# Performance work log

Measured on AMD Instinct MI355X. Metric: run time of the kernel, lower is better.

The kernel has to match this reference:

```python
import jax, jax.numpy as jnp
import numpy as np

E = 1024       # embedding_dim
HQ = 16        # num_q_heads
G = 4          # group_size
HK = HQ // G   # num_kv_heads = 4
D = E // HQ    # q_head_dim = 64
B, N = 2, 2048


def setup_inputs() -> dict:
    key = jax.random.key(0)
    kx, kq, kk, kv, ko = jax.random.split(key, 5)
    scale = 0.02
    return {
        "x": jax.random.normal(kx, (B, N, E), dtype=jnp.float32),
        # weights stored as (in, out); torch Linear computes x @ W.T, equivalent math
        "Wq": jax.random.normal(kq, (E, E), dtype=jnp.float32) * scale,
        "Wk": jax.random.normal(kk, (E, E // G), dtype=jnp.float32) * scale,
        "Wv": jax.random.normal(kv, (E, E // G), dtype=jnp.float32) * scale,
        "Wo": jax.random.normal(ko, (E, E), dtype=jnp.float32) * scale,
    }


def reference(x, Wq, Wk, Wv, Wo):
    b, n, _ = x.shape
    q = x @ Wq                      # (b, n, E)
    k = x @ Wk                      # (b, n, HK*D)
    v = x @ Wv                      # (b, n, HK*D)
    # 'b n (h d) -> b h n d' then 'b (h g) n d -> b g h n d'  (h outer, g inner)
    q = q.reshape(b, n, HQ, D).transpose(0, 2, 1, 3)          # (b, HQ, n, D)
    q = q.reshape(b, HK, G, n, D).transpose(0, 2, 1, 3, 4)    # (b, G, HK, n, D)
    k = k.reshape(b, n, HK, D).transpose(0, 2, 1, 3)          # (b, HK, n, D)
    v = v.reshape(b, n, HK, D).transpose(0, 2, 1, 3)          # (b, HK, n, D)

    scores = jnp.einsum('bghnd,bhsd->bghns', q, k) / jnp.sqrt(jnp.float32(D))
    causal = jnp.triu(jnp.ones((n, n), dtype=bool), k=1)      # True above diagonal
    scores = jnp.where(causal[None, None, None], -jnp.inf, scores)
    probs = jax.nn.softmax(scores, axis=-1)                   # dropout p=0 -> no-op
    out = jnp.einsum('bghns,bhsd->bghnd', probs, v)           # (b, G, HK, n, D)
    # 'b g h n d -> b n (h g) d -> b n (h g d)'
    out = out.transpose(0, 3, 2, 1, 4).reshape(b, n, E)
    return out @ Wo
```

## Files before the change

kernel.cpp:

```cpp
#include <hip/hip_runtime.h>
#include <hip/hip_bf16.h>
#include <math.h>

#define Bsz 2
#define Nseq 2048
#define Edim 1024
#define HQ 16
#define HK 4
#define Dh 64
#define ROWS (Bsz * Nseq)
#define QKVW 1536
#define SCL 0.1803368801111244f

typedef __attribute__((ext_vector_type(8))) short short8;
typedef __attribute__((ext_vector_type(4))) float f32x4;

__device__ __forceinline__ ushort f2bf_u(float f) {
    union { __hip_bfloat16 h; ushort u; } c;
    c.h = __float2bfloat16(f);
    return c.u;
}
__device__ __forceinline__ unsigned bfpk(float lo, float hi) {
    return ((unsigned)f2bf_u(hi) << 16) | (unsigned)f2bf_u(lo);
}

__device__ __forceinline__ void gld16(const void* g, void* l) {
    __builtin_amdgcn_global_load_lds(
        (const __attribute__((address_space(1))) unsigned*)g,
        (__attribute__((address_space(3))) unsigned*)l, 16, 0, 0);
}

__global__ __launch_bounds__(256) void castx(const float* __restrict__ x,
                                             ushort* __restrict__ xb) {
    size_t i = ((size_t)blockIdx.x * 256 + threadIdx.x) * 8;
    float4 a = *(const float4*)(x + i);
    float4 c = *(const float4*)(x + i + 4);
    short8 v;
    v[0] = f2bf_u(a.x); v[1] = f2bf_u(a.y); v[2] = f2bf_u(a.z); v[3] = f2bf_u(a.w);
    v[4] = f2bf_u(c.x); v[5] = f2bf_u(c.y); v[6] = f2bf_u(c.z); v[7] = f2bf_u(c.w);
    *(short8*)(xb + i) = v;
}

__global__ __launch_bounds__(256) void tcastAll(const float* __restrict__ Wq,
                                                const float* __restrict__ Wk,
                                                const float* __restrict__ Wv,
                                                const float* __restrict__ Wo,
                                                ushort* __restrict__ WqkvT,
                                                ushort* __restrict__ WoT) {
    __shared__ float tle[32][33];
    int bid = blockIdx.x;
    const float* src; ushort* dst; int N;
    if (bid < 1024)      { src = Wq; dst = WqkvT;                          N = 1024; }
    else if (bid < 1280) { src = Wk; dst = WqkvT + (size_t)1024 * 1024;    N = 256;  bid -= 1024; }
    else if (bid < 1536) { src = Wv; dst = WqkvT + (size_t)1280 * 1024;    N = 256;  bid -= 1280; }
    else                 { src = Wo; dst = WoT;                            N = 1024; bid -= 1536; }
    int nj = N >> 5;
    int j0 = (bid % nj) * 32, k0 = (bid / nj) * 32;
    int tx = threadIdx.x & 31, ty = threadIdx.x >> 5;
#pragma unroll
    for (int i = ty; i < 32; i += 8)
        tle[i][tx] = src[(size_t)(k0 + i) * N + j0 + tx];
    __syncthreads();
#pragma unroll
    for (int i = ty; i < 32; i += 8)
        dst[(size_t)(j0 + i) * 1024 + k0 + tx] = f2bf_u(tle[tx][i]);
}

template<int WRITE_BF16>
__global__ __launch_bounds__(256) void gemm_bt(const ushort* __restrict__ A,
                                               const ushort* __restrict__ BT,
                                               void* __restrict__ Cout,
                                               int M, int N, int K) {
    __shared__ __attribute__((aligned(16))) ushort As[2][4][128][8];
    __shared__ __attribute__((aligned(16))) ushort Bs[2][4][64][8];
    const int tid = threadIdx.x;
    const int l = tid & 63, li = l & 15, lg = l >> 4;
    const int w = tid >> 6;
    const int wr = w >> 1, wc = w & 1;
    const int row0 = blockIdx.y * 128, col0 = blockIdx.x * 64;

    f32x4 acc[4][2];
#pragma unroll
    for (int i = 0; i < 4; ++i)
#pragma unroll
        for (int j = 0; j < 2; ++j) {
            acc[i][j][0] = 0.f; acc[i][j][1] = 0.f;
            acc[i][j][2] = 0.f; acc[i][j][3] = 0.f;
        }

    const int nk = K >> 5;

#define G_STAGE(buf, kk)                                                        \
    {                                                                           \
        int k0 = (kk) << 5;                                                     \
        _Pragma("unroll")                                                       \
        for (int i = 0; i < 3; ++i) {                                           \
            int id = w + i * 4;                                                 \
            if (id < 8) {                                                       \
                int g = id >> 1, h = id & 1;                                    \
                gld16(A + (size_t)(row0 + h * 64 + l) * K + k0 + g * 8,         \
                      &As[buf][g][h * 64][0]);                                  \
            } else {                                                            \
                int g = id - 8;                                                 \
                gld16(BT + (size_t)(col0 + l) * K + k0 + g * 8,                 \
                      &Bs[buf][g][0][0]);                                       \
            }                                                                   \
        }                                                                       \
    }

    G_STAGE(0, 0);
    __syncthreads();
    int buf = 0;
    for (int kk = 0; kk < nk; ++kk) {
        if (kk + 1 < nk) G_STAGE(buf ^ 1, kk + 1);
        short8 af[4], bfr[2];
#pragma unroll
        for (int mt = 0; mt < 4; ++mt)
            af[mt] = *(const short8*)&As[buf][lg][wr * 64 + mt * 16 + li][0];
#pragma unroll
        for (int nt = 0; nt < 2; ++nt)
            bfr[nt] = *(const short8*)&Bs[buf][lg][wc * 32 + nt * 16 + li][0];
#pragma unroll
        for (int mt = 0; mt < 4; ++mt)
#pragma unroll
            for (int nt = 0; nt < 2; ++nt)
                acc[mt][nt] = __builtin_amdgcn_mfma_f32_16x16x32_bf16(
                    af[mt], bfr[nt], acc[mt][nt], 0, 0, 0);
        __syncthreads();
        buf ^= 1;
    }
#undef G_STAGE

    if (WRITE_BF16) {
        ushort* C = (ushort*)Cout;
#pragma unroll
        for (int mt = 0; mt < 4; ++mt)
#pragma unroll
            for (int r = 0; r < 4; ++r) {
                int rg = row0 + wr * 64 + mt * 16 + lg * 4 + r;
#pragma unroll
                for (int nt = 0; nt < 2; ++nt)
                    C[(size_t)rg * N + col0 + wc * 32 + nt * 16 + li] =
                        f2bf_u(acc[mt][nt][r]);
            }
    } else {
        float* C = (float*)Cout;
#pragma unroll
        for (int mt = 0; mt < 4; ++mt)
#pragma unroll
            for (int r = 0; r < 4; ++r) {
                int rg = row0 + wr * 64 + mt * 16 + lg * 4 + r;
#pragma unroll
                for (int nt = 0; nt < 2; ++nt)
                    C[(size_t)rg * N + col0 + wc * 32 + nt * 16 + li] =
                        acc[mt][nt][r];
            }
    }
}

__global__ __launch_bounds__(256) void attn_mfma(const ushort* __restrict__ qkv,
                                                 ushort* __restrict__ o) {
    __shared__ __attribute__((aligned(16))) char smem[40960];
    ushort (*Ks)[8][64][8] = (ushort (*)[8][64][8])smem;
    unsigned (*VtD)[2048]  = (unsigned (*)[2048])(smem + 16384);
    ushort (*Ps)[8][16][8] = (ushort (*)[8][16][8])(smem + 32768);

    const int tid = threadIdx.x;
    const int l = tid & 63, li = l & 15, lg = l >> 4;
    const int w = tid >> 6;
    const int bx = blockIdx.x;
    const int hq = blockIdx.y, b = blockIdx.z, hk = hq >> 2;

    const int kp = 2 * (tid & 31), d0v = (tid >> 5) * 8;
    const int gv = kp >> 3, prv = (kp & 7) >> 1;

    const ushort* base  = qkv + (size_t)b * Nseq * QKVW;
    const ushort* vbase = base + 1280 + hk * 64 + d0v;
    const int qloc = w * 16 + li;

    for (int hseg = 0; hseg < 2; ++hseg) {
        const int qt = hseg ? (31 - bx) : bx;
        const int r0 = qt * 64;

        short8 q8[2];
#pragma unroll
        for (int c = 0; c < 2; ++c)
            q8[c] = *(const short8*)(base + (size_t)(r0 + qloc) * QKVW +
                                     hq * 64 + (c * 4 + lg) * 8);

#pragma unroll
        for (int i = 0; i < 2; ++i) {
            int g = w + i * 4;
            gld16(base + (size_t)l * QKVW + 1024 + hk * 64 + g * 8,
                  &Ks[0][g][0][0]);
        }
        short8 va = *(const short8*)(vbase + (size_t)kp * QKVW);
        short8 vb = *(const short8*)(vbase + (size_t)(kp + 1) * QKVW);
        __syncthreads();
#pragma unroll
        for (int i2 = 0; i2 < 8; ++i2) {
            unsigned pv = ((unsigned)(unsigned short)va[i2]) |
                          (((unsigned)(unsigned short)vb[i2]) << 16);
            VtD[0][gv * 256 + (((d0v + i2) * 4 + prv) ^ (gv << 2))] = pv;
        }
        __syncthreads();

        f32x4 oacc[4];
#pragma unroll
        for (int dt = 0; dt < 4; ++dt) {
            oacc[dt][0] = 0.f; oacc[dt][1] = 0.f;
            oacc[dt][2] = 0.f; oacc[dt][3] = 0.f;
        }
        float m = -INFINITY, lsum = 0.f;

        for (int t = 0; t <= qt; ++t) {
            const int cur = t & 1, nxt = cur ^ 1;
            const bool pre = (t < qt);
            short8 vna, vnb;
            if (pre) {
                const int s1 = (t + 1) * 64;
#pragma unroll
                for (int i = 0; i < 2; ++i) {
                    int g = w + i * 4;
                    gld16(base + (size_t)(s1 + l) * QKVW + 1024 + hk * 64 + g * 8,
                          &Ks[nxt][g][0][0]);
                }
                const ushort* vr = vbase + (size_t)(s1 + kp) * QKVW;
                vna = *(const short8*)vr;
                vnb = *(const short8*)(vr + QKVW);
            }

            f32x4 s[4];
#pragma unroll
            for (int kb = 0; kb < 4; ++kb) {
                s[kb][0] = 0.f; s[kb][1] = 0.f; s[kb][2] = 0.f; s[kb][3] = 0.f;
            }
#pragma unroll
            for (int c = 0; c < 2; ++c)
#pragma unroll
                for (int kb = 0; kb < 4; ++kb) {
                    short8 bk = *(const short8*)&Ks[cur][c * 4 + lg][kb * 16 + li][0];
                    s[kb] = __builtin_amdgcn_mfma_f32_16x16x32_bf16(bk, q8[c], s[kb], 0, 0, 0);
                }

            float p[16];
            const bool last = (t == qt);
#pragma unroll
            for (int kb = 0; kb < 4; ++kb)
#pragma unroll
                for (int r = 0; r < 4; ++r) {
                    float sv = s[kb][r] * SCL;
                    if (last && (kb * 16 + lg * 4 + r > qloc)) sv = -INFINITY;
                    p[kb * 4 + r] = sv;
                }

            float mx = p[0];
#pragma unroll
            for (int i = 1; i < 16; ++i) mx = fmaxf(mx, p[i]);
            mx = fmaxf(mx, __shfl_xor(mx, 16, 64));
            mx = fmaxf(mx, __shfl_xor(mx, 32, 64));
            float mn = fmaxf(m, mx);
            float al = exp2f(m - mn);
            float sum = 0.f;
#pragma unroll
            for (int i = 0; i < 16; ++i) {
                float e = exp2f(p[i] - mn);
                p[i] = e;
                sum += e;
            }
            sum += __shfl_xor(sum, 16, 64);
            sum += __shfl_xor(sum, 32, 64);
            m = mn;
            lsum = lsum * al + sum;

            float alr[4];
#pragma unroll
            for (int r = 0; r < 4; ++r) alr[r] = __shfl(al, lg * 4 + r, 64);
#pragma unroll
            for (int dt = 0; dt < 4; ++dt)
#pragma unroll
                for (int r = 0; r < 4; ++r) oacc[dt][r] *= alr[r];

#pragma unroll
            for (int kb = 0; kb < 4; ++kb) {
                unsigned lo = bfpk(p[kb * 4 + 0], p[kb * 4 + 1]);
                unsigned hi = bfpk(p[kb * 4 + 2], p[kb * 4 + 3]);
                *(unsigned long long*)&Ps[w][2 * kb + (lg >> 1)][li][(lg & 1) * 4] =
                    ((unsigned long long)hi << 32) | (unsigned long long)lo;
            }

            if (pre) {
#pragma unroll
                for (int i2 = 0; i2 < 8; ++i2) {
                    unsigned pv = ((unsigned)(unsigned short)vna[i2]) |
                                  (((unsigned)(unsigned short)vnb[i2]) << 16);
                    VtD[nxt][gv * 256 + (((d0v + i2) * 4 + prv) ^ (gv << 2))] = pv;
                }
            }

#pragma unroll
            for (int c = 0; c < 2; ++c) {
                short8 pa = *(const short8*)&Ps[w][c * 4 + lg][li][0];
#pragma unroll
                for (int dt = 0; dt < 4; ++dt) {
                    int g = c * 4 + lg, d = dt * 16 + li;
                    short8 bv = *(const short8*)(&VtD[cur][g * 256 + ((d * 4) ^ (g << 2))]);
                    oacc[dt] = __builtin_amdgcn_mfma_f32_16x16x32_bf16(pa, bv, oacc[dt], 0, 0, 0);
                }
            }
            __syncthreads();
        }

        float linv[4];
#pragma unroll
        for (int r = 0; r < 4; ++r) linv[r] = 1.0f / __shfl(lsum, lg * 4 + r, 64);
#pragma unroll
        for (int r = 0; r < 4; ++r) {
            int rg = b * Nseq + r0 + w * 16 + lg * 4 + r;
#pragma unroll
            for (int dt = 0; dt < 4; ++dt)
                o[(size_t)rg * Edim + hq * 64 + dt * 16 + li] =
                    f2bf_u(oacc[dt][r] * linv[r]);
        }
    }
}

extern "C" void kernel_launch(void* const* d_in, const int* in_sizes, int n_in,
                              void* d_out, int out_size, void* d_ws, size_t ws_size,
                              hipStream_t stream) {
    const float* x  = (const float*)d_in[0];
    const float* Wq = (const float*)d_in[1];
    const float* Wk = (const float*)d_in[2];
    const float* Wv = (const float*)d_in[3];
    const float* Wo = (const float*)d_in[4];

    ushort* ws    = (ushort*)d_ws;
    ushort* xb    = ws;
    ushort* WqkvT = xb + (size_t)ROWS * Edim;
    ushort* WoT   = WqkvT + (size_t)QKVW * Edim;
    ushort* qkv   = WoT + (size_t)Edim * Edim;
    ushort* at    = qkv + (size_t)ROWS * QKVW;

    castx<<<ROWS * Edim / (256 * 8), 256, 0, stream>>>(x, xb);
    tcastAll<<<2560, 256, 0, stream>>>(Wq, Wk, Wv, Wo, WqkvT, WoT);

    gemm_bt<1><<<dim3(QKVW / 64, ROWS / 128), 256, 0, stream>>>(
        xb, WqkvT, qkv, ROWS, QKVW, Edim);

    attn_mfma<<<dim3(Nseq / 128, HQ, Bsz), 256, 0, stream>>>(qkv, at);

    gemm_bt<0><<<dim3(Edim / 64, ROWS / 128), 256, 0, stream>>>(
        at, WoT, d_out, ROWS, Edim, Edim);
}
```

Measured before the change: 211.2 us.

## Fold softmax scale into Wq, lazy rescale online softmax, perm-based V packing

Folds the log2e/sqrt(D) softmax scale into the bf16 cast of Wq so the attention loop skips a per-score multiply. Online softmax now rescales the output accumulator and running max only when some lane's max grows by more than 8 (log2 domain), which removes most exp2 and shuffle-multiply work on the common path. V transpose packing uses v_perm byte permutes instead of per-element shifts and ors, and the max reduction becomes a balanced tree. The trade-off is that the lazily updated max lets exponents reach up to 2^8, a small numerical risk, and scaling Wq before the bf16 cast changes rounding slightly.

```diff
diff --git a/kernel.cpp b/kernel.cpp
--- a/kernel.cpp
+++ b/kernel.cpp
@@ -15,6 +15,8 @@
 typedef __attribute__((ext_vector_type(8))) short short8;
 typedef __attribute__((ext_vector_type(4))) float f32x4;
 
+union S8U { short8 s8; unsigned u[4]; };
+
 __device__ __forceinline__ ushort f2bf_u(float f) {
     union { __hip_bfloat16 h; ushort u; } c;
     c.h = __float2bfloat16(f);
@@ -49,8 +51,8 @@
                                                 ushort* __restrict__ WoT) {
     __shared__ float tle[32][33];
     int bid = blockIdx.x;
-    const float* src; ushort* dst; int N;
-    if (bid < 1024)      { src = Wq; dst = WqkvT;                          N = 1024; }
+    const float* src; ushort* dst; int N; float sc = 1.0f;
+    if (bid < 1024)      { src = Wq; dst = WqkvT;                          N = 1024; sc = SCL; }
     else if (bid < 1280) { src = Wk; dst = WqkvT + (size_t)1024 * 1024;    N = 256;  bid -= 1024; }
     else if (bid < 1536) { src = Wv; dst = WqkvT + (size_t)1280 * 1024;    N = 256;  bid -= 1280; }
     else                 { src = Wo; dst = WoT;                            N = 1024; bid -= 1536; }
@@ -63,7 +65,7 @@
     __syncthreads();
 #pragma unroll
     for (int i = ty; i < 32; i += 8)
-        dst[(size_t)(j0 + i) * 1024 + k0 + tx] = f2bf_u(tle[tx][i]);
+        dst[(size_t)(j0 + i) * 1024 + k0 + tx] = f2bf_u(tle[tx][i] * sc);
 }
 
 template<int WRITE_BF16>
@@ -197,11 +199,15 @@
         short8 va = *(const short8*)(vbase + (size_t)kp * QKVW);
         short8 vb = *(const short8*)(vbase + (size_t)(kp + 1) * QKVW);
         __syncthreads();
-#pragma unroll
-        for (int i2 = 0; i2 < 8; ++i2) {
-            unsigned pv = ((unsigned)(unsigned short)va[i2]) |
-                          (((unsigned)(unsigned short)vb[i2]) << 16);
-            VtD[0][gv * 256 + (((d0v + i2) * 4 + prv) ^ (gv << 2))] = pv;
+        {
+            S8U ua, ub; ua.s8 = va; ub.s8 = vb;
+#pragma unroll
+            for (int j = 0; j < 4; ++j) {
+                VtD[0][gv * 256 + (((d0v + 2 * j) * 4 + prv) ^ (gv << 2))] =
+                    __builtin_amdgcn_perm(ub.u[j], ua.u[j], 0x05040100u);
+                VtD[0][gv * 256 + (((d0v + 2 * j + 1) * 4 + prv) ^ (gv << 2))] =
+                    __builtin_amdgcn_perm(ub.u[j], ua.u[j], 0x07060302u);
+            }
         }
         __syncthreads();
 
@@ -249,37 +255,43 @@
             for (int kb = 0; kb < 4; ++kb)
 #pragma unroll
                 for (int r = 0; r < 4; ++r) {
-                    float sv = s[kb][r] * SCL;
+                    float sv = s[kb][r];
                     if (last && (kb * 16 + lg * 4 + r > qloc)) sv = -INFINITY;
                     p[kb * 4 + r] = sv;
                 }
 
-            float mx = p[0];
-#pragma unroll
-            for (int i = 1; i < 16; ++i) mx = fmaxf(mx, p[i]);
+            float mx = fmaxf(fmaxf(
+                fmaxf(fmaxf(p[0], p[1]), fmaxf(p[2], p[3])),
+                fmaxf(fmaxf(p[4], p[5]), fmaxf(p[6], p[7]))),
+                fmaxf(fmaxf(fmaxf(p[8], p[9]), fmaxf(p[10], p[11])),
+                      fmaxf(fmaxf(p[12], p[13]), fmaxf(p[14], p[15]))));
             mx = fmaxf(mx, __shfl_xor(mx, 16, 64));
             mx = fmaxf(mx, __shfl_xor(mx, 32, 64));
-            float mn = fmaxf(m, mx);
-            float al = exp2f(m - mn);
+
+            if (__any(mx - m > 8.0f)) {
+                float mn = fmaxf(m, mx);
+                float al = exp2f(m - mn);
+                m = mn;
+                lsum *= al;
+                float alr[4];
+#pragma unroll
+                for (int r = 0; r < 4; ++r) alr[r] = __shfl(al, lg * 4 + r, 64);
+#pragma unroll
+                for (int dt = 0; dt < 4; ++dt)
+#pragma unroll
+                    for (int r = 0; r < 4; ++r) oacc[dt][r] *= alr[r];
+            }
+
             float sum = 0.f;
 #pragma unroll
             for (int i = 0; i < 16; ++i) {
-                float e = exp2f(p[i] - mn);
+                float e = exp2f(p[i] - m);
                 p[i] = e;
                 sum += e;
             }
             sum += __shfl_xor(sum, 16, 64);
             sum += __shfl_xor(sum, 32, 64);
-            m = mn;
-            lsum = lsum * al + sum;
-
-            float alr[4];
-#pragma unroll
-            for (int r = 0; r < 4; ++r) alr[r] = __shfl(al, lg * 4 + r, 64);
-#pragma unroll
-            for (int dt = 0; dt < 4; ++dt)
-#pragma unroll
-                for (int r = 0; r < 4; ++r) oacc[dt][r] *= alr[r];
+            lsum += sum;
 
 #pragma unroll
             for (int kb = 0; kb < 4; ++kb) {
@@ -290,11 +302,13 @@
             }
 
             if (pre) {
-#pragma unroll
-                for (int i2 = 0; i2 < 8; ++i2) {
-                    unsigned pv = ((unsigned)(unsigned short)vna[i2]) |
-                                  (((unsigned)(unsigned short)vnb[i2]) << 16);
-                    VtD[nxt][gv * 256 + (((d0v + i2) * 4 + prv) ^ (gv << 2))] = pv;
+                S8U ua, ub; ua.s8 = vna; ub.s8 = vnb;
+#pragma unroll
+                for (int j = 0; j < 4; ++j) {
+                    VtD[nxt][gv * 256 + (((d0v + 2 * j) * 4 + prv) ^ (gv << 2))] =
+                        __builtin_amdgcn_perm(ub.u[j], ua.u[j], 0x05040100u);
+                    VtD[nxt][gv * 256 + (((d0v + 2 * j + 1) * 4 + prv) ^ (gv << 2))] =
+                        __builtin_amdgcn_perm(ub.u[j], ua.u[j], 0x07060302u);
                 }
             }
 
```

New measurement: 209.3 us. Within noise of the previous version (-0.9%).
